# Performance work log

Hardware: AMD Instinct MI355X
Metric: run time of the kernel (lower is better)

The kernel has to match this reference:

```python
import jax, jax.numpy as jnp
import numpy as np

D, B, V = 8, 4096, 1024          # token fields (type..section), batch streams, vocab per field
THRES = 0.9                      # top_k filter_thres default
TEMP = 1.0                       # temperature default
NOTE_TYPE = 1                    # note_type_code; sos=0, eos=2


def setup_inputs() -> dict:
    key = jax.random.key(0)
    k1, k2, k3 = jax.random.split(key, 3)
    logits = jax.random.normal(k1, (D, B, V), dtype=jnp.float32)
    u = jax.random.uniform(k2, (D, B, V), dtype=jnp.float32)
    current_values = jax.random.randint(k3, (D, B), 0, 16).astype(jnp.int32)
    return {"logits": logits, "u": u, "current_values": current_values}


def reference(logits, u, current_values):
    neg = -jnp.inf
    ar = jnp.arange(V)
    # monotonicity mask: positions < current value are forbidden  [D,B,V]
    lg = jnp.where(ar[None, None, :] < current_values[:, :, None], neg, logits)
    # index 0 is masked for every field (logits[d][:, 0] = -inf in the loop)
    lg = lg.at[:, :, 0].set(neg)
    # top-k filtering: keep values >= k-th largest, k = int((1 - thres) * V)
    k = int((1.0 - THRES) * V)
    kth = jax.lax.top_k(lg, k)[0][..., -1:]          # [D,B,1]
    filt = jnp.where(lg < kth, neg, lg)
    logp = jax.nn.log_softmax(filt / TEMP, axis=-1)  # stable softmax, -inf -> prob 0
    probs = jnp.exp(logp)
    # multinomial sampling via Gumbel-max using provided uniform noise
    eps = 1e-20
    gumbel = -jnp.log(-jnp.log(u + eps) + eps)
    samples = jnp.argmax(logp + gumbel, axis=-1)     # [D,B]
    # type-conditional fill: fields 1..7 are zero unless sampled type == NOTE
    is_note = samples[0] == NOTE_TYPE                # [B]
    keep = (jnp.arange(D)[:, None] == 0) | is_note[None, :]
    tokens = jnp.where(keep, samples, 0)             # [D,B]
    return tokens.T, probs                           # [B,D] int, [D,B,V] float
```

## Files before the change

### kernel.cpp

```cpp
#include <hip/hip_runtime.h>
#include <math.h>

#define DD 8
#define BB 4096
#define VV 1024
#define K_SEL 102
#define RPB 4

__device__ __forceinline__ unsigned f2key(float f) {
    unsigned u = __float_as_uint(f);
    unsigned m = (unsigned)((int)u >> 31) | 0x80000000u;
    return u ^ m;
}
__device__ __forceinline__ float key2f(unsigned k) {
    unsigned m = 0x80000000u | ~((unsigned)((int)k >> 31));
    return __uint_as_float(k ^ m);
}

__global__ __launch_bounds__(256) void decode_row_kernel(
    const float* __restrict__ logits,
    const float* __restrict__ unoise,
    const int* __restrict__ curvals,
    float* __restrict__ probs_out,
    int* __restrict__ samples)
{
    const int wave = threadIdx.x >> 6;
    const int lane = threadIdx.x & 63;
    const int row  = blockIdx.x * RPB + wave;

    __shared__ __align__(16) unsigned hist[RPB][1040];
    unsigned* h = hist[wave];

    const float4* l4 = (const float4*)(logits + (size_t)row * VV);
    const float4* u4 = (const float4*)(unoise + (size_t)row * VV);
    const int cv1 = max(curvals[row], 1);

    unsigned key[16];
    float    fv[16];
#pragma unroll
    for (int i = 0; i < 4; i++) {
        float4 ff = l4[i * 64 + lane];
        const int vb = i * 256 + lane * 4;
        float e[4] = {ff.x, ff.y, ff.z, ff.w};
#pragma unroll
        for (int j = 0; j < 4; j++) {
            int v = vb + j;
            float t = (v < cv1) ? -INFINITY : e[j];
            fv[i * 4 + j]  = t;
            key[i * 4 + j] = f2key(t);
        }
    }

    unsigned prefix = 0;
    unsigned kk = K_SEL;
    const int rep = (lane & 3) * 260;
#pragma unroll
    for (int pass = 0; pass < 2; pass++) {
        const int shift = 24 - 8 * pass;
        const uint4 z = {0u, 0u, 0u, 0u};
#pragma unroll
        for (int r = 0; r < 4; r++)
            ((uint4*)(h + r * 260))[lane] = z;
        __builtin_amdgcn_wave_barrier();
#pragma unroll
        for (int i = 0; i < 16; i++) {
            unsigned t = (key[i] ^ prefix) >> shift;
            unsigned inc = (pass == 0) ? 1u : (t < 256u ? 1u : 0u);
            atomicAdd(h + rep + (t & 0xFFu), inc);
        }
        __threadfence_block();
        __builtin_amdgcn_wave_barrier();
        uint4 c0 = ((uint4*)(h + 0 * 260))[lane];
        uint4 c1 = ((uint4*)(h + 1 * 260))[lane];
        uint4 c2 = ((uint4*)(h + 2 * 260))[lane];
        uint4 c3 = ((uint4*)(h + 3 * 260))[lane];
        __builtin_amdgcn_wave_barrier();
        unsigned cnt0 = c0.x + c1.x + c2.x + c3.x;
        unsigned cnt1 = c0.y + c1.y + c2.y + c3.y;
        unsigned cnt2 = c0.z + c1.z + c2.z + c3.z;
        unsigned cnt3 = c0.w + c1.w + c2.w + c3.w;
        unsigned s3 = cnt3;
        unsigned s2 = cnt2 + s3;
        unsigned s1 = cnt1 + s2;
        unsigned s0 = cnt0 + s1;
        unsigned suf = s0;
#pragma unroll
        for (int off = 1; off < 64; off <<= 1) {
            unsigned o = __shfl_down(suf, off, 64);
            suf += (lane + off < 64) ? o : 0u;
        }
        const unsigned above = suf - s0;
        unsigned sel = 0u;
        bool found = false;
        {
            unsigned ge, gt;
            ge = s0 + above; gt = ge - cnt0;
            if (ge >= kk && gt < kk) { found = true; sel = ((unsigned)(lane * 4 + 0) << 16) | (kk - gt); }
            ge = s1 + above; gt = ge - cnt1;
            if (ge >= kk && gt < kk) { found = true; sel = ((unsigned)(lane * 4 + 1) << 16) | (kk - gt); }
            ge = s2 + above; gt = ge - cnt2;
            if (ge >= kk && gt < kk) { found = true; sel = ((unsigned)(lane * 4 + 2) << 16) | (kk - gt); }
            ge = s3 + above; gt = ge - cnt3;
            if (ge >= kk && gt < kk) { found = true; sel = ((unsigned)(lane * 4 + 3) << 16) | (kk - gt); }
        }
        unsigned long long bal = __ballot(found);
        int src = __ffsll((unsigned long long)bal) - 1;
        sel = __shfl(sel, src, 64);
        prefix |= (sel >> 16) << shift;
        kk = sel & 0xFFFFu;
        __builtin_amdgcn_wave_barrier();
    }

    unsigned cmask = 0u;
#pragma unroll
    for (int i = 0; i < 16; i++)
        if ((key[i] & 0xFFFF0000u) == prefix) cmask |= (1u << i);
    unsigned thr;
    for (;;) {
        unsigned mx = 0u;
#pragma unroll
        for (int i = 0; i < 16; i++)
            if (cmask & (1u << i)) mx = max(mx, key[i]);
#pragma unroll
        for (int off = 32; off; off >>= 1)
            mx = max(mx, (unsigned)__shfl_xor((int)mx, off, 64));
        if (kk <= 1u) { thr = mx; break; }
        unsigned ceq = 0u;
#pragma unroll
        for (int i = 0; i < 16; i++)
            if (key[i] == mx) ceq++;
#pragma unroll
        for (int off = 32; off; off >>= 1)
            ceq += (unsigned)__shfl_xor((int)ceq, off, 64);
        if (kk <= ceq) { thr = mx; break; }
        kk -= ceq;
#pragma unroll
        for (int i = 0; i < 16; i++)
            if (key[i] == mx) cmask &= ~(1u << i);
    }
    const float thrf = key2f(thr);

    float m = fv[0];
#pragma unroll
    for (int i = 1; i < 16; i++) m = fmaxf(m, fv[i]);
#pragma unroll
    for (int off = 32; off; off >>= 1)
        m = fmaxf(m, __shfl_xor(m, off, 64));

    float ex[16];
    float s = 0.0f;
#pragma unroll
    for (int i = 0; i < 16; i++) {
        float e = (fv[i] >= thrf) ? __expf(fv[i] - m) : 0.0f;
        ex[i] = e;
        s += e;
    }
    float4 uu[4];
#pragma unroll
    for (int i = 0; i < 4; i++) uu[i] = u4[i * 64 + lane];
#pragma unroll
    for (int off = 32; off; off >>= 1)
        s += __shfl_xor(s, off, 64);
    const float inv = 1.0f / s;

    float bnum = 0.0f, bden = 1.0f;
    int   besti = VV;
    float4* p4 = (float4*)(probs_out + (size_t)row * VV);
#pragma unroll
    for (int i = 0; i < 4; i++) {
        float4 pv;
        pv.x = ex[i * 4 + 0] * inv;
        pv.y = ex[i * 4 + 1] * inv;
        pv.z = ex[i * 4 + 2] * inv;
        pv.w = ex[i * 4 + 3] * inv;
        p4[i * 64 + lane] = pv;
        float us[4] = {uu[i].x, uu[i].y, uu[i].z, uu[i].w};
#pragma unroll
        for (int j = 0; j < 4; j++) {
            const int idx = i * 4 + j;
            float nl = 1e-20f - __logf(us[j] + 1e-20f);
            float a  = ex[idx];
            int v = i * 256 + lane * 4 + j;
            if (a * bden > bnum * nl) { bnum = a; bden = nl; besti = v; }
        }
    }
#pragma unroll
    for (int off = 32; off; off >>= 1) {
        float onum = __shfl_xor(bnum, off, 64);
        float oden = __shfl_xor(bden, off, 64);
        int   oi   = __shfl_xor(besti, off, 64);
        float x = onum * bden, y = bnum * oden;
        if (x > y || (x == y && oi < besti)) { bnum = onum; bden = oden; besti = oi; }
    }
    if (lane == 0) samples[row] = besti;
}

__global__ __launch_bounds__(256) void tokens_kernel(
    const int* __restrict__ samples, float* __restrict__ tokens_out)
{
    int i = blockIdx.x * 256 + threadIdx.x;
    int b = i >> 3;
    int d = i & 7;
    int sm = samples[d * BB + b];
    int t0 = samples[b];
    tokens_out[i] = (d == 0 || t0 == 1) ? (float)sm : 0.0f;
}

extern "C" void kernel_launch(void* const* d_in, const int* in_sizes, int n_in,
                              void* d_out, int out_size, void* d_ws, size_t ws_size,
                              hipStream_t stream) {
    const float* logits = (const float*)d_in[0];
    const float* unoise = (const float*)d_in[1];
    const int*   curvals = (const int*)d_in[2];

    float* out        = (float*)d_out;
    float* tokens_out = out;
    float* probs_out  = out + (size_t)BB * DD;
    int*   samples    = (int*)d_ws;

    decode_row_kernel<<<(DD * BB) / RPB, 256, 0, stream>>>(logits, unoise, curvals,
                                                           probs_out, samples);
    tokens_kernel<<<(BB * DD) / 256, 256, 0, stream>>>(samples, tokens_out);
}
```

Before: 317.0 us.

## Replace LDS histogram radix select with ballot-based bitwise radix select

Swaps the two-pass 8-bit shared-memory histogram top-k threshold search for a 16-step bit-by-bit radix select. Each step counts matching keys with wave ballots and popcounts, so no LDS atomics, zeroing or prefix scans are needed. It also drops the separate float copies and recovers floats from the sortable keys, which cuts register pressure. The cost is 16 sequential steps of 16 ballots each, more instructions on what may be a memory-bound path.

```diff
diff --git a/kernel.cpp b/kernel.cpp
--- a/kernel.cpp
+++ b/kernel.cpp
@@ -6,6 +6,7 @@
 #define VV 1024
 #define K_SEL 102
 #define RPB 4
+#define TOPBITS 16
 
 __device__ __forceinline__ unsigned f2key(float f) {
     unsigned u = __float_as_uint(f);
@@ -28,15 +29,11 @@
     const int lane = threadIdx.x & 63;
     const int row  = blockIdx.x * RPB + wave;
 
-    __shared__ __align__(16) unsigned hist[RPB][1040];
-    unsigned* h = hist[wave];
-
     const float4* l4 = (const float4*)(logits + (size_t)row * VV);
     const float4* u4 = (const float4*)(unoise + (size_t)row * VV);
     const int cv1 = max(curvals[row], 1);
 
     unsigned key[16];
-    float    fv[16];
 #pragma unroll
     for (int i = 0; i < 4; i++) {
         float4 ff = l4[i * 64 + lane];
@@ -44,77 +41,29 @@
         float e[4] = {ff.x, ff.y, ff.z, ff.w};
 #pragma unroll
         for (int j = 0; j < 4; j++) {
-            int v = vb + j;
-            float t = (v < cv1) ? -INFINITY : e[j];
-            fv[i * 4 + j]  = t;
+            float t = (vb + j < cv1) ? -INFINITY : e[j];
             key[i * 4 + j] = f2key(t);
         }
     }
 
-    unsigned prefix = 0;
+    unsigned p  = 0u;
     unsigned kk = K_SEL;
-    const int rep = (lane & 3) * 260;
 #pragma unroll
-    for (int pass = 0; pass < 2; pass++) {
-        const int shift = 24 - 8 * pass;
-        const uint4 z = {0u, 0u, 0u, 0u};
+    for (int b = 31; b >= 32 - TOPBITS; --b) {
+        const unsigned tgt = (p >> b) | 1u;
+        unsigned n = 0;
 #pragma unroll
-        for (int r = 0; r < 4; r++)
-            ((uint4*)(h + r * 260))[lane] = z;
-        __builtin_amdgcn_wave_barrier();
-#pragma unroll
-        for (int i = 0; i < 16; i++) {
-            unsigned t = (key[i] ^ prefix) >> shift;
-            unsigned inc = (pass == 0) ? 1u : (t < 256u ? 1u : 0u);
-            atomicAdd(h + rep + (t & 0xFFu), inc);
-        }
-        __threadfence_block();
-        __builtin_amdgcn_wave_barrier();
-        uint4 c0 = ((uint4*)(h + 0 * 260))[lane];
-        uint4 c1 = ((uint4*)(h + 1 * 260))[lane];
-        uint4 c2 = ((uint4*)(h + 2 * 260))[lane];
-        uint4 c3 = ((uint4*)(h + 3 * 260))[lane];
-        __builtin_amdgcn_wave_barrier();
-        unsigned cnt0 = c0.x + c1.x + c2.x + c3.x;
-        unsigned cnt1 = c0.y + c1.y + c2.y + c3.y;
-        unsigned cnt2 = c0.z + c1.z + c2.z + c3.z;
-        unsigned cnt3 = c0.w + c1.w + c2.w + c3.w;
-        unsigned s3 = cnt3;
-        unsigned s2 = cnt2 + s3;
-        unsigned s1 = cnt1 + s2;
-        unsigned s0 = cnt0 + s1;
-        unsigned suf = s0;
-#pragma unroll
-        for (int off = 1; off < 64; off <<= 1) {
-            unsigned o = __shfl_down(suf, off, 64);
-            suf += (lane + off < 64) ? o : 0u;
-        }
-        const unsigned above = suf - s0;
-        unsigned sel = 0u;
-        bool found = false;
-        {
-            unsigned ge, gt;
-            ge = s0 + above; gt = ge - cnt0;
-            if (ge >= kk && gt < kk) { found = true; sel = ((unsigned)(lane * 4 + 0) << 16) | (kk - gt); }
-            ge = s1 + above; gt = ge - cnt1;
-            if (ge >= kk && gt < kk) { found = true; sel = ((unsigned)(lane * 4 + 1) << 16) | (kk - gt); }
-            ge = s2 + above; gt = ge - cnt2;
-            if (ge >= kk && gt < kk) { found = true; sel = ((unsigned)(lane * 4 + 2) << 16) | (kk - gt); }
-            ge = s3 + above; gt = ge - cnt3;
-            if (ge >= kk && gt < kk) { found = true; sel = ((unsigned)(lane * 4 + 3) << 16) | (kk - gt); }
-        }
-        unsigned long long bal = __ballot(found);
-        int src = __ffsll((unsigned long long)bal) - 1;
-        sel = __shfl(sel, src, 64);
-        prefix |= (sel >> 16) << shift;
-        kk = sel & 0xFFFFu;
-        __builtin_amdgcn_wave_barrier();
+        for (int i = 0; i < 16; i++)
+            n += (unsigned)__popcll(__ballot((key[i] >> b) == tgt));
+        if (n >= kk) p |= (1u << b);
+        else         kk -= n;
     }
 
+    const unsigned PMASK = ~((1u << (32 - TOPBITS)) - 1u);
     unsigned cmask = 0u;
 #pragma unroll
     for (int i = 0; i < 16; i++)
-        if ((key[i] & 0xFFFF0000u) == prefix) cmask |= (1u << i);
+        if ((key[i] & PMASK) == p) cmask |= (1u << i);
     unsigned thr;
     for (;;) {
         unsigned mx = 0u;
@@ -128,30 +77,27 @@
         unsigned ceq = 0u;
 #pragma unroll
         for (int i = 0; i < 16; i++)
-            if (key[i] == mx) ceq++;
-#pragma unroll
-        for (int off = 32; off; off >>= 1)
-            ceq += (unsigned)__shfl_xor((int)ceq, off, 64);
+            ceq += (unsigned)__popcll(__ballot(key[i] == mx));
         if (kk <= ceq) { thr = mx; break; }
         kk -= ceq;
 #pragma unroll
         for (int i = 0; i < 16; i++)
             if (key[i] == mx) cmask &= ~(1u << i);
     }
-    const float thrf = key2f(thr);
 
-    float m = fv[0];
+    unsigned mk = key[0];
 #pragma unroll
-    for (int i = 1; i < 16; i++) m = fmaxf(m, fv[i]);
+    for (int i = 1; i < 16; i++) mk = max(mk, key[i]);
 #pragma unroll
     for (int off = 32; off; off >>= 1)
-        m = fmaxf(m, __shfl_xor(m, off, 64));
+        mk = max(mk, (unsigned)__shfl_xor((int)mk, off, 64));
+    const float m = key2f(mk);
 
     float ex[16];
     float s = 0.0f;
 #pragma unroll
     for (int i = 0; i < 16; i++) {
-        float e = (fv[i] >= thrf) ? __expf(fv[i] - m) : 0.0f;
+        float e = (key[i] >= thr) ? __expf(key2f(key[i]) - m) : 0.0f;
         ex[i] = e;
         s += e;
     }
```

Result: no change. 318.4 us (+0.4%).
